# Performance work log

Hardware: AMD Instinct MI355X
Metric: run time of the kernel (lower is better)

The kernel has to match this reference:

```python
import jax, jax.numpy as jnp
import numpy as np

UP = 512      # up_size
RADIUS = 60   # revise crop radius -> 120x120 squares
COEF = 1.5    # COM threshold coefficient
DOT = 4       # intensity-adjust circle radius
B = 16
M = 4
BASE = 128


def _affine_grid(theta, H, W):
    # torch F.affine_grid, align_corners=False. theta: (2,3) -> grid (H,W,2) with (x,y)
    xs = (2.0 * jnp.arange(W, dtype=jnp.float32) + 1.0) / W - 1.0
    ys = (2.0 * jnp.arange(H, dtype=jnp.float32) + 1.0) / H - 1.0
    X, Y = jnp.meshgrid(xs, ys)  # (H,W), X varies along width
    base = jnp.stack([X, Y, jnp.ones_like(X)], axis=-1)  # (H,W,3)
    return base @ theta.T  # (H,W,2)


def _gs_one(im, gr):
    # torch F.grid_sample, bilinear, zero padding, align_corners=False
    # im: (C,H,W), gr: (Hg,Wg,2) -> (C,Hg,Wg)
    C, H, W = im.shape
    x = ((gr[..., 0] + 1.0) * W - 1.0) * 0.5
    y = ((gr[..., 1] + 1.0) * H - 1.0) * 0.5
    x0 = jnp.floor(x)
    y0 = jnp.floor(y)
    wx = x - x0
    wy = y - y0

    def tap(ix, iy, w):
        valid = (ix >= 0) & (ix < W) & (iy >= 0) & (iy < H)
        ii = jnp.clip(iy, 0, H - 1).astype(jnp.int32)
        jj = jnp.clip(ix, 0, W - 1).astype(jnp.int32)
        return im[:, ii, jj] * (jnp.where(valid, w, 0.0))[None]

    return (tap(x0, y0, (1 - wx) * (1 - wy))
            + tap(x0 + 1, y0, wx * (1 - wy))
            + tap(x0, y0 + 1, (1 - wx) * wy)
            + tap(x0 + 1, y0 + 1, wx * wy))


_grid_sample = jax.vmap(_gs_one)  # (B,C,H,W),(B,Hg,Wg,2)->(B,C,Hg,Wg)


def _inv2x3(theta):
    # append [0,0,1], invert 3x3, keep top 2 rows (as in Joint.forward)
    n = theta.shape[0]
    bottom = jnp.broadcast_to(jnp.array([[0.0, 0.0, 1.0]], jnp.float32), (n, 1, 3))
    full = jnp.concatenate([theta, bottom], axis=1)
    return jnp.linalg.inv(full)[:, :2]


def _com(img, mask, coef):
    # center_of_mass: threshold = coef * mean over mask, intensity-weighted centroid
    H, W = img.shape
    msum = jnp.maximum(mask.sum(), 1.0)
    thr = (img.sum() / msum) * coef
    w = jnp.where(img > thr, img, 0.0)
    tot = w.sum() + 1e-8
    cx = (w.sum(axis=1) * jnp.arange(H, dtype=img.dtype)).sum() / tot  # row
    cy = (w.sum(axis=0) * jnp.arange(W, dtype=img.dtype)).sum() / tot  # col
    return cx, cy


def _revise(image, masks_rot, inv_theta, adj, radius, coef, dot):
    # revise_size_on_affine_gpu with adj_para given and pare_reverse=True
    d = 2 * radius
    yy, xx = jnp.meshgrid(jnp.arange(d), jnp.arange(d), indexing='ij')
    small_sq = ((yy - radius) ** 2 + (xx - radius) ** 2) <= dot ** 2  # dot mask

    def per_item(img_i, new_i, mask_i, th_i, a_i):
        cx, cy = _com(new_i, mask_i, coef)
        x0 = jnp.round(cx).astype(jnp.int32) - radius
        y0 = jnp.round(cy).astype(jnp.int32) - radius
        small = jax.lax.dynamic_slice(img_i[0], (x0, y0), (d, d))
        small = jnp.where(small_sq, small / a_i, small)  # pare_reverse=True -> divide
        out = _gs_one(small[None], _affine_grid(th_i, d, d))  # (1,d,d)
        return jax.lax.dynamic_update_slice(img_i, out, (0, x0, y0))

    img = image
    for j in range(masks_rot.shape[0]):
        mj = masks_rot[j]                 # (B,H,W) float 0/1
        new = image[:, 0] * mj            # COM always from original image*mask
        img = jax.vmap(per_item)(img, new, mj, inv_theta, adj)
    return img


def setup_inputs() -> dict:
    key = jax.random.key(0)
    ks = jax.random.split(key, 6)
    predicted_base = jax.random.uniform(ks[0], (B, 1, BASE, BASE), jnp.float32)
    e = 0.05 * jax.random.normal(ks[1], (B, 4), jnp.float32)
    sc = (jnp.zeros((B, 2, 3), jnp.float32)
          .at[:, 0, 0].set(1.0 + e[:, 0]).at[:, 0, 1].set(e[:, 1])
          .at[:, 1, 0].set(e[:, 2]).at[:, 1, 1].set(1.0 + e[:, 3]))
    ang = jax.random.uniform(ks[2], (B,), jnp.float32, -0.2, 0.2)
    rot = (jnp.zeros((B, 2, 3), jnp.float32)
           .at[:, 0, 0].set(jnp.cos(ang)).at[:, 0, 1].set(-jnp.sin(ang))
           .at[:, 1, 0].set(jnp.sin(ang)).at[:, 1, 1].set(jnp.cos(ang)))
    t = jax.random.uniform(ks[3], (B, 2), jnp.float32, -0.05, 0.05)
    tr = (jnp.zeros((B, 2, 3), jnp.float32)
          .at[:, 0, 0].set(1.0).at[:, 1, 1].set(1.0)
          .at[:, 0, 2].set(t[:, 0]).at[:, 1, 2].set(t[:, 1]))
    adj = jax.random.uniform(ks[4], (B,), jnp.float32, 0.9, 1.1)
    centers = [(128, 128), (128, 384), (384, 128), (384, 384)]
    yy, xx = np.meshgrid(np.arange(UP), np.arange(UP), indexing='ij')
    masks = np.stack([((yy - cy) ** 2 + (xx - cx) ** 2 <= 30 ** 2).astype(np.float32)
                      for (cy, cx) in centers])
    return dict(predicted_base=predicted_base, scaler_shear=sc, rotation=rot,
                translation=tr, adj_mask=adj, masks=jnp.asarray(masks))


def reference(predicted_base, scaler_shear, rotation, translation, adj_mask, masks):
    b = predicted_base.shape[0]
    it1 = _inv2x3(scaler_shear)
    it2 = _inv2x3(rotation)
    it3 = _inv2x3(translation)
    base_inp = jax.image.resize(predicted_base, (b, 1, UP, UP), method='linear')
    mk_grid = jax.vmap(lambda th: _affine_grid(th, UP, UP))
    g1, g2, g3 = mk_grid(it1), mk_grid(it2), mk_grid(it3)
    pred_trans = _grid_sample(base_inp, g3)
    pred_rot = _grid_sample(pred_trans, g2)
    pred_input = _grid_sample(pred_rot, g1)
    # rotate masks through grid_2 then grid_1, threshold at 0.5
    new_masks = []
    for j in range(masks.shape[0]):
        bm = jnp.broadcast_to(masks[j][None, None], (b, 1, UP, UP))
        rm = _grid_sample(_grid_sample(bm, g2), g1)
        new_masks.append(rm[:, 0] >= 0.5)
    masks_rot = jnp.stack(new_masks)  # (M,B,UP,UP) bool
    pred_revise = _revise(pred_input, masks_rot.astype(pred_input.dtype), it1,
                          adj_mask, RADIUS, COEF, DOT)
    return (base_inp, pred_input, pred_revise, masks_rot)
```

## Files before the change

kernel.cpp:

```cpp
#include <hip/hip_runtime.h>
#include <math.h>
#include <limits.h>

#define NPIX (512*512)
#define NB 16
#define RAD 60
#define DSZ 120
#define PSTR 121
#define GTS 48
#define GSTR 49


__device__ __forceinline__ float gs_bilinear(const float* img, int H, int W,
                                             float gx, float gy) {
    float x = ((gx + 1.0f) * (float)W - 1.0f) * 0.5f;
    float y = ((gy + 1.0f) * (float)H - 1.0f) * 0.5f;
    float xf = floorf(x), yf = floorf(y);
    int ix = (int)xf, iy = (int)yf;
    float wx = x - xf, wy = y - yf;
    float v = 0.0f;
    bool vx0 = (ix >= 0) && (ix < W);
    bool vx1 = (ix >= -1) && (ix < W - 1);
    bool vy0 = (iy >= 0) && (iy < H);
    bool vy1 = (iy >= -1) && (iy < H - 1);
    if (vx0 && vy0) v += img[iy*W + ix]         * ((1.0f - wx) * (1.0f - wy));
    if (vx1 && vy0) v += img[iy*W + ix + 1]     * (wx * (1.0f - wy));
    if (vx0 && vy1) v += img[(iy+1)*W + ix]     * ((1.0f - wx) * wy);
    if (vx1 && vy1) v += img[(iy+1)*W + ix + 1] * (wx * wy);
    return v;
}

__device__ __forceinline__ float gs_bilinear_patch(const float* img, float gx, float gy) {
    float x = ((gx + 1.0f) * 120.0f - 1.0f) * 0.5f;
    float y = ((gy + 1.0f) * 120.0f - 1.0f) * 0.5f;
    float xf = floorf(x), yf = floorf(y);
    int ix = (int)xf, iy = (int)yf;
    float wx = x - xf, wy = y - yf;
    float v = 0.0f;
    bool vx0 = (ix >= 0) && (ix < 120);
    bool vx1 = (ix >= -1) && (ix < 119);
    bool vy0 = (iy >= 0) && (iy < 120);
    bool vy1 = (iy >= -1) && (iy < 119);
    if (vx0 && vy0) v += img[iy*PSTR + ix]         * ((1.0f - wx) * (1.0f - wy));
    if (vx1 && vy0) v += img[iy*PSTR + ix + 1]     * (wx * (1.0f - wy));
    if (vx0 && vy1) v += img[(iy+1)*PSTR + ix]     * ((1.0f - wx) * wy);
    if (vx1 && vy1) v += img[(iy+1)*PSTR + ix + 1] * (wx * wy);
    return v;
}


__global__ void k_prep(const float* __restrict__ sc, const float* __restrict__ rot,
                       const float* __restrict__ tr, float* __restrict__ ws_inv,
                       int* __restrict__ bbox, unsigned* __restrict__ occ,
                       int* __restrict__ qcount) {
    int t = threadIdx.x;
    if (t < 48) {
        int m = t >> 4, b = t & 15;
        const float* th = (m == 0 ? sc : (m == 1 ? rot : tr)) + b * 6;
        float a  = th[0], bb = th[1], tx = th[2];
        float c  = th[3], d  = th[4], ty = th[5];
        float L10 = c / a;
        float dp  = d  - L10 * bb;
        float typ = ty - L10 * tx;
        float i10 = (0.0f - L10) / dp;
        float i00 = (1.0f - bb * i10) / a;
        float i11 = 1.0f / dp;
        float i01 = (0.0f - bb * i11) / a;
        float i12 = (0.0f - typ) / dp;
        float i02 = (0.0f - bb * i12 - tx) / a;
        float* o = ws_inv + m * 96 + b * 6;
        o[0] = i00; o[1] = i01; o[2] = i02;
        o[3] = i10; o[4] = i11; o[5] = i12;
    }
    bbox[t] = ((t & 3) < 2) ? INT_MAX : INT_MIN;
    if (t < 128) occ[t] = 0u;
    if (t == 0) *qcount = 0;
}

__global__ void __launch_bounds__(256) k_occ(const float* __restrict__ masks,
                                             unsigned* __restrict__ occ) {
    int tile = blockIdx.x * 4 + (threadIdx.x >> 6);
    int lane = threadIdx.x & 63;
    int j = tile >> 10, t = tile & 1023;
    int ty = t >> 5, tx = t & 31;
    const float* mk = masks + (size_t)j * NPIX;
    int any = 0;
    for (int i = lane; i < 256; i += 64) {
        int py = ty * 16 + (i >> 4), px = tx * 16 + (i & 15);
        if (mk[py * 512 + px] != 0.0f) any = 1;
    }
    unsigned long long m = __ballot(any);
    if (lane == 0 && m) atomicOr(&occ[j * 32 + ty], 1u << tx);
}

__global__ void __launch_bounds__(256) k_otile(const unsigned* __restrict__ occ,
                                               const float* __restrict__ inv1,
                                               const float* __restrict__ inv2,
                                               int* __restrict__ queue,
                                               int* __restrict__ qcount) {
    int idx = blockIdx.x * 256 + threadIdx.x;
    int jb = idx >> 10, tile = idx & 1023;
    int j = jb >> 4, b = jb & 15;
    int ty = tile >> 5, tx = tile & 31;
    const float* t1 = inv1 + b * 6;
    const float* t2 = inv2 + b * 6;
    float xs[2] = { (float)(tx * 16), (float)(tx * 16 + 15) };
    float ys[2] = { (float)(ty * 16), (float)(ty * 16 + 15) };
    float sxmin = 1e30f, sxmax = -1e30f, symin = 1e30f, symax = -1e30f;
    for (int cy = 0; cy < 2; ++cy)
        for (int cx = 0; cx < 2; ++cx) {
            float X = (2.0f * xs[cx] + 1.0f) / 512.0f - 1.0f;
            float Y = (2.0f * ys[cy] + 1.0f) / 512.0f - 1.0f;
            float gx = t1[0] * X + t1[1] * Y + t1[2];
            float gy = t1[3] * X + t1[4] * Y + t1[5];
            float sx = ((gx + 1.0f) * 512.0f - 1.0f) * 0.5f;
            float sy = ((gy + 1.0f) * 512.0f - 1.0f) * 0.5f;
            sxmin = fminf(sxmin, sx); sxmax = fmaxf(sxmax, sx);
            symin = fminf(symin, sy); symax = fmaxf(symax, sy);
        }
    int c0 = max((int)floorf(sxmin) - 1, 0), c1 = min((int)floorf(sxmax) + 2, 511);
    int r0 = max((int)floorf(symin) - 1, 0), r1 = min((int)floorf(symax) + 2, 511);
    bool any = false;
    if (c0 <= c1 && r0 <= r1) {
        float A0 = t2[0], A1 = t2[1], A3 = t2[3], A4 = t2[4];
        float Kx = 0.5f * (-511.0f * (A0 + A1) + 512.0f * t2[2] + 511.0f);
        float Ky = 0.5f * (-511.0f * (A3 + A4) + 512.0f * t2[5] + 511.0f);
        float pxmin = A0 * (A0 >= 0.f ? c0 : c1) + A1 * (A1 >= 0.f ? r0 : r1) + Kx;
        float pxmax = A0 * (A0 >= 0.f ? c1 : c0) + A1 * (A1 >= 0.f ? r1 : r0) + Kx;
        float pymin = A3 * (A3 >= 0.f ? c0 : c1) + A4 * (A4 >= 0.f ? r0 : r1) + Ky;
        float pymax = A3 * (A3 >= 0.f ? c1 : c0) + A4 * (A4 >= 0.f ? r1 : r0) + Ky;
        int xlo = max((int)floorf(pxmin) - 1, 0), xhi = min((int)floorf(pxmax) + 2, 511);
        int ylo = max((int)floorf(pymin) - 1, 0), yhi = min((int)floorf(pymax) + 2, 511);
        if (xlo <= xhi && ylo <= yhi)
            for (int tr = ylo >> 4; tr <= yhi >> 4; ++tr)
                for (int tc = xlo >> 4; tc <= xhi >> 4; ++tc)
                    if ((occ[j * 32 + tr] >> tc) & 1u) any = true;
    }
    if (any) {
        int pos = atomicAdd(qcount, 1);
        queue[pos] = (jb << 10) | tile;
    }
}

__global__ void __launch_bounds__(256) k_zero(float4* __restrict__ p, int n4) {
    int stride = gridDim.x * 256;
    for (int i = blockIdx.x * 256 + threadIdx.x; i < n4; i += stride)
        p[i] = make_float4(0.f, 0.f, 0.f, 0.f);
}

__global__ void __launch_bounds__(256) k_upsample(const float* __restrict__ in,
                                                  float* __restrict__ out) {
    int b = blockIdx.y;
    int p4 = blockIdx.x * 256 + threadIdx.x;
    int p = p4 * 4;
    int y = p >> 9, x0p = p & 511;
    const float* src = in + b * 128 * 128;
    float r[4];
    float sy = (float)y * 0.25f - 0.375f;
    float fy0 = floorf(sy);
    int iy = (int)fy0;
    float fy = sy - fy0;
    int iy0 = min(max(iy, 0), 127), iy1 = min(max(iy + 1, 0), 127);
    #pragma unroll
    for (int k = 0; k < 4; ++k) {
        int x = x0p + k;
        float sx = (float)x * 0.25f - 0.375f;
        float fx0 = floorf(sx);
        int ix = (int)fx0;
        float fx = sx - fx0;
        int ix0 = min(max(ix, 0), 127), ix1 = min(max(ix + 1, 0), 127);
        float v00 = src[iy0 * 128 + ix0], v10 = src[iy0 * 128 + ix1];
        float v01 = src[iy1 * 128 + ix0], v11 = src[iy1 * 128 + ix1];
        r[k] = (v00 * (1.0f - fx) + v10 * fx) * (1.0f - fy)
             + (v01 * (1.0f - fx) + v11 * fx) * fy;
    }
    *(float4*)(out + (size_t)b * NPIX + p) = make_float4(r[0], r[1], r[2], r[3]);
}

__global__ void __launch_bounds__(256) k_gsample(const float* __restrict__ src,
                                                 float* __restrict__ dst,
                                                 float* __restrict__ dst2,
                                                 const float* __restrict__ thetas) {
    __shared__ float tb[GTS * GSTR];
    int b = blockIdx.y;
    int tile = blockIdx.x;
    int ox = (tile & 15) * 32, oy = (tile >> 4) * 32;
    const float* th = thetas + b * 6;
    float t0 = th[0], t1 = th[1], t2 = th[2], t3 = th[3], t4 = th[4], t5 = th[5];
    const float* im = src + (size_t)b * NPIX;

    float sxmin = 1e30f, sxmax = -1e30f, symin = 1e30f, symax = -1e30f;
    #pragma unroll
    for (int cy = 0; cy < 2; ++cy)
        #pragma unroll
        for (int cx = 0; cx < 2; ++cx) {
            float X = (2.0f * (float)(ox + cx * 31) + 1.0f) / 512.0f - 1.0f;
            float Y = (2.0f * (float)(oy + cy * 31) + 1.0f) / 512.0f - 1.0f;
            float gx = t0 * X + t1 * Y + t2;
            float gy = t3 * X + t4 * Y + t5;
            float sx = ((gx + 1.0f) * 512.0f - 1.0f) * 0.5f;
            float sy = ((gy + 1.0f) * 512.0f - 1.0f) * 0.5f;
            sxmin = fminf(sxmin, sx); sxmax = fmaxf(sxmax, sx);
            symin = fminf(symin, sy); symax = fmaxf(symax, sy);
        }
    int rx0 = (int)floorf(sxmin) - 1;
    int ry0 = (int)floorf(symin) - 1;
    bool fits = ((int)floorf(sxmax) + 2 - rx0 < GTS) &&
                ((int)floorf(symax) + 2 - ry0 < GTS);

    int t = threadIdx.x;
    int py = oy + (t >> 3);
    int px0 = ox + (t & 7) * 4;
    float Y = (2.0f * (float)py + 1.0f) / 512.0f - 1.0f;
    float r[4];

    if (fits) {
        for (int i = t; i < GTS * GTS; i += 256) {
            int rr = i / GTS, cc = i - rr * GTS;
            int gy_ = ry0 + rr, gx_ = rx0 + cc;
            float v = 0.0f;
            if (gx_ >= 0 && gx_ < 512 && gy_ >= 0 && gy_ < 512)
                v = im[gy_ * 512 + gx_];
            tb[rr * GSTR + cc] = v;
        }
        __syncthreads();
        #pragma unroll
        for (int k = 0; k < 4; ++k) {
            float X = (2.0f * (float)(px0 + k) + 1.0f) / 512.0f - 1.0f;
            float gx = t0 * X + t1 * Y + t2;
            float gy = t3 * X + t4 * Y + t5;
            float x = ((gx + 1.0f) * 512.0f - 1.0f) * 0.5f;
            float y = ((gy + 1.0f) * 512.0f - 1.0f) * 0.5f;
            float xf = floorf(x), yf = floorf(y);
            int ix = (int)xf, iy = (int)yf;
            float wx = x - xf, wy = y - yf;
            int lx = ix - rx0, ly = iy - ry0;
            float v;
            v  = tb[ly * GSTR + lx]           * ((1.0f - wx) * (1.0f - wy));
            v += tb[ly * GSTR + lx + 1]       * (wx * (1.0f - wy));
            v += tb[(ly + 1) * GSTR + lx]     * ((1.0f - wx) * wy);
            v += tb[(ly + 1) * GSTR + lx + 1] * (wx * wy);
            r[k] = v;
        }
    } else {
        #pragma unroll
        for (int k = 0; k < 4; ++k) {
            float X = (2.0f * (float)(px0 + k) + 1.0f) / 512.0f - 1.0f;
            float gx = t0 * X + t1 * Y + t2;
            float gy = t3 * X + t4 * Y + t5;
            r[k] = gs_bilinear(im, 512, 512, gx, gy);
        }
    }
    float4 v4 = make_float4(r[0], r[1], r[2], r[3]);
    size_t op = (size_t)b * NPIX + py * 512 + px0;
    *(float4*)(dst + op) = v4;
    if (dst2) *(float4*)(dst2 + op) = v4;
}

__device__ __forceinline__ float rm2_val(const float* mk, const float* t2, int cx_, int ry_) {
    float X2 = (2.0f * (float)cx_ + 1.0f) / 512.0f - 1.0f;
    float Y2 = (2.0f * (float)ry_ + 1.0f) / 512.0f - 1.0f;
    float g2x = t2[0] * X2 + t2[1] * Y2 + t2[2];
    float g2y = t2[3] * X2 + t2[4] * Y2 + t2[5];
    return gs_bilinear(mk, 512, 512, g2x, g2y);
}

__global__ void __launch_bounds__(256) k_mask_live(const float* __restrict__ masks,
                                                   float* __restrict__ out3,
                                                   const float* __restrict__ inv1,
                                                   const float* __restrict__ inv2,
                                                   const int* __restrict__ queue,
                                                   const int* __restrict__ qcount,
                                                   int* __restrict__ bbox) {
    __shared__ int sbb[4];
    int n = *qcount;
    for (int q = blockIdx.x; q < n; q += gridDim.x) {
        int e = queue[q];
        int jb = e >> 10, tile = e & 1023;
        if (threadIdx.x == 0) { sbb[0] = INT_MAX; sbb[1] = INT_MAX; sbb[2] = INT_MIN; sbb[3] = INT_MIN; }
        __syncthreads();

        int ty = tile >> 5, tx = tile & 31;
        int y = ty * 16 + (threadIdx.x >> 4);
        int x = tx * 16 + (threadIdx.x & 15);
        int j = jb >> 4, b = jb & 15;
        const float* t1 = inv1 + b * 6;
        const float* t2 = inv2 + b * 6;
        const float* mk = masks + (size_t)j * NPIX;

        float X = (2.0f * (float)x + 1.0f) / 512.0f - 1.0f;
        float Y = (2.0f * (float)y + 1.0f) / 512.0f - 1.0f;
        float gx = t1[0] * X + t1[1] * Y + t1[2];
        float gy = t1[3] * X + t1[4] * Y + t1[5];
        float sx = ((gx + 1.0f) * 512.0f - 1.0f) * 0.5f;
        float sy = ((gy + 1.0f) * 512.0f - 1.0f) * 0.5f;
        float xf = floorf(sx), yf = floorf(sy);
        int ix = (int)xf, iy = (int)yf;
        float wx = sx - xf, wy = sy - yf;

        float v = 0.0f;
        bool vx0 = (ix >= 0) && (ix < 512);
        bool vx1 = (ix >= -1) && (ix < 511);
        bool vy0 = (iy >= 0) && (iy < 512);
        bool vy1 = (iy >= -1) && (iy < 511);
        if (vx0 && vy0) v += rm2_val(mk, t2, ix,     iy    ) * ((1.0f - wx) * (1.0f - wy));
        if (vx1 && vy0) v += rm2_val(mk, t2, ix + 1, iy    ) * (wx * (1.0f - wy));
        if (vx0 && vy1) v += rm2_val(mk, t2, ix,     iy + 1) * ((1.0f - wx) * wy);
        if (vx1 && vy1) v += rm2_val(mk, t2, ix + 1, iy + 1) * (wx * wy);

        float res = 0.0f;
        if (v >= 0.5f) {
            res = 1.0f;
            atomicMin(&sbb[0], y); atomicMin(&sbb[1], x);
            atomicMax(&sbb[2], y); atomicMax(&sbb[3], x);
        }
        out3[(size_t)jb * NPIX + y * 512 + x] = res;

        __syncthreads();
        if (threadIdx.x == 0 && sbb[2] != INT_MIN) {
            atomicMin(&bbox[jb * 4 + 0], sbb[0]);
            atomicMin(&bbox[jb * 4 + 1], sbb[1]);
            atomicMax(&bbox[jb * 4 + 2], sbb[2]);
            atomicMax(&bbox[jb * 4 + 3], sbb[3]);
        }
        __syncthreads();
    }
}

__global__ void __launch_bounds__(256) k_stats(const float* __restrict__ pred,
                                               const float* __restrict__ mrot,
                                               const int* __restrict__ bbox,
                                               int* __restrict__ xy) {
    int jb = blockIdx.x;
    int b = jb & 15;
    int rmin = bbox[jb*4+0], cmin = bbox[jb*4+1], rmax = bbox[jb*4+2], cmax = bbox[jb*4+3];
    const float* img = pred + (size_t)b * NPIX;
    const float* mk  = mrot + (size_t)jb * NPIX;
    int lane = threadIdx.x & 63, w = threadIdx.x >> 6;
    int W = cmax - cmin + 1;
    int total = (rmax >= rmin) ? W * (rmax - rmin + 1) : 0;

    double msum = 0.0, isum = 0.0;
    for (int i = threadIdx.x; i < total; i += 256) {
        int r = rmin + i / W, c = cmin + i % W;
        float m = mk[r * 512 + c];
        if (m != 0.0f) {
            msum += (double)m;
            isum += (double)(img[r * 512 + c] * m);
        }
    }
    for (int o = 32; o > 0; o >>= 1) {
        msum += __shfl_down(msum, o, 64);
        isum += __shfl_down(isum, o, 64);
    }
    __shared__ double s0[4], s1[4], s2[4];
    __shared__ double sthr;
    if (lane == 0) { s0[w] = msum; s1[w] = isum; }
    __syncthreads();
    if (threadIdx.x == 0) {
        double M = s0[0] + s0[1] + s0[2] + s0[3];
        double I = s1[0] + s1[1] + s1[2] + s1[3];
        sthr = (I / fmax(M, 1.0)) * 1.5;
    }
    __syncthreads();
    double t = sthr;

    double wsum = 0.0, sy = 0.0, sx = 0.0;
    for (int i = threadIdx.x; i < total; i += 256) {
        int r = rmin + i / W, c = cmin + i % W;
        float m = mk[r * 512 + c];
        if (m != 0.0f) {
            float v = img[r * 512 + c] * m;
            if ((double)v > t) {
                double vd = (double)v;
                wsum += vd;
                sy += vd * (double)r;
                sx += vd * (double)c;
            }
        }
    }
    for (int o = 32; o > 0; o >>= 1) {
        wsum += __shfl_down(wsum, o, 64);
        sy   += __shfl_down(sy,   o, 64);
        sx   += __shfl_down(sx,   o, 64);
    }
    __syncthreads();
    if (lane == 0) { s0[w] = wsum; s1[w] = sy; s2[w] = sx; }
    __syncthreads();
    if (threadIdx.x == 0) {
        double W_ = s0[0] + s0[1] + s0[2] + s0[3];
        double SY = s1[0] + s1[1] + s1[2] + s1[3];
        double SX = s2[0] + s2[1] + s2[2] + s2[3];
        double tot = W_ + 1e-8;
        int x0 = (int)rint(SY / tot) - RAD;
        int y0 = (int)rint(SX / tot) - RAD;
        x0 = min(max(x0, 0), 512 - DSZ);
        y0 = min(max(y0, 0), 512 - DSZ);
        xy[jb * 2 + 0] = x0;
        xy[jb * 2 + 1] = y0;
    }
}

__device__ __forceinline__ void patch_one(float* __restrict__ im, float* __restrict__ patch,
                                          int x0, int y0, float a,
                                          float t0, float t1, float t2,
                                          float t3, float t4, float t5) {
    for (int t = threadIdx.x; t < DSZ * DSZ; t += 1024) {
        int u = t / DSZ, v = t % DSZ;
        float val = im[(x0 + u) * 512 + (y0 + v)];
        int du = u - RAD, dv = v - RAD;
        if (du * du + dv * dv <= 16) val = val / a;
        patch[u * PSTR + v] = val;
    }
    __syncthreads();
    for (int t = threadIdx.x; t < DSZ * DSZ; t += 1024) {
        int py = t / DSZ, px = t % DSZ;
        float X = (2.0f * (float)px + 1.0f) / 120.0f - 1.0f;
        float Y = (2.0f * (float)py + 1.0f) / 120.0f - 1.0f;
        float gx = t0 * X + t1 * Y + t2;
        float gy = t3 * X + t4 * Y + t5;
        float o = gs_bilinear_patch(patch, gx, gy);
        im[(x0 + py) * 512 + (y0 + px)] = o;
    }
}

__global__ void __launch_bounds__(1024) k_patch(float* __restrict__ img,
                                                const int* __restrict__ xy,
                                                const float* __restrict__ inv1,
                                                const float* __restrict__ adj) {
    __shared__ float patch[DSZ * PSTR];
    int b = blockIdx.x >> 2, j = blockIdx.x & 3;
    int rx[4], ry[4];
    #pragma unroll
    for (int k = 0; k < 4; ++k) {
        rx[k] = xy[(k * 16 + b) * 2 + 0];
        ry[k] = xy[(k * 16 + b) * 2 + 1];
    }
    bool overlap = false;
    #pragma unroll
    for (int i = 0; i < 4; ++i)
        #pragma unroll
        for (int k = 0; k < 4; ++k)
            if (i < k && abs(rx[i] - rx[k]) < DSZ && abs(ry[i] - ry[k]) < DSZ)
                overlap = true;

    float a = adj[b];
    float* im = img + (size_t)b * NPIX;
    const float* th = inv1 + b * 6;
    float t0 = th[0], t1 = th[1], t2 = th[2], t3 = th[3], t4 = th[4], t5 = th[5];

    if (!overlap) {
        patch_one(im, patch, rx[j], ry[j], a, t0, t1, t2, t3, t4, t5);
    } else {
        if (j != 0) return;
        for (int jj = 0; jj < 4; ++jj) {
            patch_one(im, patch, rx[jj], ry[jj], a, t0, t1, t2, t3, t4, t5);
            __threadfence_block();
            __syncthreads();
        }
    }
}


extern "C" void kernel_launch(void* const* d_in, const int* in_sizes, int n_in,
                              void* d_out, int out_size, void* d_ws, size_t ws_size,
                              hipStream_t stream) {
    const float* base  = (const float*)d_in[0];
    const float* sc    = (const float*)d_in[1];
    const float* rot   = (const float*)d_in[2];
    const float* tr    = (const float*)d_in[3];
    const float* adj   = (const float*)d_in[4];
    const float* masks = (const float*)d_in[5];

    float* out  = (float*)d_out;
    float* out0 = out;
    float* out1 = out0 + (size_t)NB * NPIX;
    float* out2 = out1 + (size_t)NB * NPIX;
    float* out3 = out2 + (size_t)NB * NPIX;

    float*    inv1   = (float*)d_ws;
    float*    inv2   = inv1 + 96;
    float*    inv3   = inv1 + 192;
    int*      xy     = (int*)((char*)d_ws + 4096);
    int*      bbox   = (int*)((char*)d_ws + 8192);
    unsigned* occ    = (unsigned*)((char*)d_ws + 12288);
    int*      qcount = (int*)((char*)d_ws + 16128);
    int*      queue  = (int*)((char*)d_ws + 16384);

    dim3 gridUp(256, NB);
    dim3 gridTile(256, NB);

    k_prep<<<1, 256, 0, stream>>>(sc, rot, tr, (float*)d_ws, bbox, occ, qcount);
    k_occ<<<1024, 256, 0, stream>>>(masks, occ);
    k_otile<<<256, 256, 0, stream>>>(occ, inv1, inv2, queue, qcount);
    k_upsample<<<gridUp, 256, 0, stream>>>(base, out0);

    k_gsample<<<gridTile, 256, 0, stream>>>(out0, out2, nullptr, inv3);
    k_gsample<<<gridTile, 256, 0, stream>>>(out2, out3, nullptr, inv2);
    k_gsample<<<gridTile, 256, 0, stream>>>(out3, out1, out2, inv1);

    k_zero<<<2048, 256, 0, stream>>>((float4*)out3, 64 * NPIX / 4);
    k_mask_live<<<1024, 256, 0, stream>>>(masks, out3, inv1, inv2, queue, qcount, bbox);

    k_stats<<<64, 256, 0, stream>>>(out1, out3, bbox, xy);

    k_patch<<<64, 1024, 0, stream>>>(out2, xy, inv1, adj);
}
```

Baseline: 247.0 us.

## Merge prep, occupancy, upsample and tile-queue kernels; skip zeroing live mask tiles

Combines the independent setup work (theta inversion, mask occupancy bitmap, upsampling) into one kernel split by block index, and puts the output-tile liveness test into the first grid-sample launch. Occupancy words are now built with one vectorized wave per row instead of per-tile atomics. The zero-fill is merged with the live-mask kernel and writes only tiles that no live block will overwrite, using a new per-tile flag array. This cuts the launch count from about eleven to seven and removes redundant zero writes to the mask output, in exchange for branchy mixed-role kernels and an extra byte-flag array.

```diff
diff --git a/kernel.cpp b/kernel.cpp
--- a/kernel.cpp
+++ b/kernel.cpp
@@ -48,57 +48,181 @@
     return v;
 }
 
-
-__global__ void k_prep(const float* __restrict__ sc, const float* __restrict__ rot,
-                       const float* __restrict__ tr, float* __restrict__ ws_inv,
-                       int* __restrict__ bbox, unsigned* __restrict__ occ,
-                       int* __restrict__ qcount) {
+__global__ void __launch_bounds__(256) k_init(const float* __restrict__ base,
+                                              const float* __restrict__ sc,
+                                              const float* __restrict__ rot,
+                                              const float* __restrict__ tr,
+                                              const float* __restrict__ masks,
+                                              float* __restrict__ out0,
+                                              float* __restrict__ ws_inv,
+                                              int* __restrict__ bbox,
+                                              unsigned* __restrict__ occ,
+                                              int* __restrict__ qcount) {
+    int bid = blockIdx.x;
+    if (bid < 4096) {
+        int b = bid >> 8;
+        int p4 = (bid & 255) * 256 + threadIdx.x;
+        int p = p4 * 4;
+        int y = p >> 9, x0p = p & 511;
+        const float* src = base + b * 128 * 128;
+        float r[4];
+        float sy = (float)y * 0.25f - 0.375f;
+        float fy0 = floorf(sy);
+        int iy = (int)fy0;
+        float fy = sy - fy0;
+        int iy0 = min(max(iy, 0), 127), iy1 = min(max(iy + 1, 0), 127);
+        #pragma unroll
+        for (int k = 0; k < 4; ++k) {
+            int x = x0p + k;
+            float sx = (float)x * 0.25f - 0.375f;
+            float fx0 = floorf(sx);
+            int ix = (int)fx0;
+            float fx = sx - fx0;
+            int ix0 = min(max(ix, 0), 127), ix1 = min(max(ix + 1, 0), 127);
+            float v00 = src[iy0 * 128 + ix0], v10 = src[iy0 * 128 + ix1];
+            float v01 = src[iy1 * 128 + ix0], v11 = src[iy1 * 128 + ix1];
+            r[k] = (v00 * (1.0f - fx) + v10 * fx) * (1.0f - fy)
+                 + (v01 * (1.0f - fx) + v11 * fx) * fy;
+        }
+        *(float4*)(out0 + (size_t)b * NPIX + p) = make_float4(r[0], r[1], r[2], r[3]);
+    } else if (bid < 4128) {
+        int word = (bid - 4096) * 4 + (threadIdx.x >> 6);
+        int lane = threadIdx.x & 63;
+        int j = word >> 5, ty = word & 31;
+        const float* mk = masks + (size_t)j * NPIX + ty * 16 * 512 + lane * 8;
+        int any = 0;
+        for (int rr = 0; rr < 16; ++rr) {
+            const float4* p = (const float4*)(mk + rr * 512);
+            float4 a = p[0], c = p[1];
+            if (a.x != 0.f || a.y != 0.f || a.z != 0.f || a.w != 0.f ||
+                c.x != 0.f || c.y != 0.f || c.z != 0.f || c.w != 0.f) any = 1;
+        }
+        unsigned long long bb = __ballot(any);
+        if (lane == 0) {
+            unsigned wrd = 0;
+            for (int tx = 0; tx < 32; ++tx)
+                if (bb & (3ull << (2 * tx))) wrd |= 1u << tx;
+            occ[j * 32 + ty] = wrd;
+        }
+    } else {
+        int t = threadIdx.x;
+        if (t < 48) {
+            int m = t >> 4, b = t & 15;
+            const float* th = (m == 0 ? sc : (m == 1 ? rot : tr)) + b * 6;
+            float a  = th[0], bbv = th[1], tx = th[2];
+            float c  = th[3], d   = th[4], ty = th[5];
+            float L10 = c / a;
+            float dp  = d  - L10 * bbv;
+            float typ = ty - L10 * tx;
+            float i10 = (0.0f - L10) / dp;
+            float i00 = (1.0f - bbv * i10) / a;
+            float i11 = 1.0f / dp;
+            float i01 = (0.0f - bbv * i11) / a;
+            float i12 = (0.0f - typ) / dp;
+            float i02 = (0.0f - bbv * i12 - tx) / a;
+            float* o = ws_inv + m * 96 + b * 6;
+            o[0] = i00; o[1] = i01; o[2] = i02;
+            o[3] = i10; o[4] = i11; o[5] = i12;
+        }
+        bbox[t] = ((t & 3) < 2) ? INT_MAX : INT_MIN;
+        if (t == 0) *qcount = 0;
+    }
+}
+
+__device__ __forceinline__ void gsample_tile(const float* __restrict__ src,
+                                             float* __restrict__ dst,
+                                             float* __restrict__ dst2,
+                                             const float* __restrict__ thetas,
+                                             int b, int tile, float* tb) {
+    int ox = (tile & 15) * 32, oy = (tile >> 4) * 32;
+    const float* th = thetas + b * 6;
+    float t0 = th[0], t1 = th[1], t2 = th[2], t3 = th[3], t4 = th[4], t5 = th[5];
+    const float* im = src + (size_t)b * NPIX;
+
+    float sxmin = 1e30f, sxmax = -1e30f, symin = 1e30f, symax = -1e30f;
+    #pragma unroll
+    for (int cy = 0; cy < 2; ++cy)
+        #pragma unroll
+        for (int cx = 0; cx < 2; ++cx) {
+            float X = (2.0f * (float)(ox + cx * 31) + 1.0f) / 512.0f - 1.0f;
+            float Y = (2.0f * (float)(oy + cy * 31) + 1.0f) / 512.0f - 1.0f;
+            float gx = t0 * X + t1 * Y + t2;
+            float gy = t3 * X + t4 * Y + t5;
+            float sx = ((gx + 1.0f) * 512.0f - 1.0f) * 0.5f;
+            float sy = ((gy + 1.0f) * 512.0f - 1.0f) * 0.5f;
+            sxmin = fminf(sxmin, sx); sxmax = fmaxf(sxmax, sx);
+            symin = fminf(symin, sy); symax = fmaxf(symax, sy);
+        }
+    int rx0 = (int)floorf(sxmin) - 1;
+    int ry0 = (int)floorf(symin) - 1;
+    bool fits = ((int)floorf(sxmax) + 2 - rx0 < GTS) &&
+                ((int)floorf(symax) + 2 - ry0 < GTS);
+
     int t = threadIdx.x;
-    if (t < 48) {
-        int m = t >> 4, b = t & 15;
-        const float* th = (m == 0 ? sc : (m == 1 ? rot : tr)) + b * 6;
-        float a  = th[0], bb = th[1], tx = th[2];
-        float c  = th[3], d  = th[4], ty = th[5];
-        float L10 = c / a;
-        float dp  = d  - L10 * bb;
-        float typ = ty - L10 * tx;
-        float i10 = (0.0f - L10) / dp;
-        float i00 = (1.0f - bb * i10) / a;
-        float i11 = 1.0f / dp;
-        float i01 = (0.0f - bb * i11) / a;
-        float i12 = (0.0f - typ) / dp;
-        float i02 = (0.0f - bb * i12 - tx) / a;
-        float* o = ws_inv + m * 96 + b * 6;
-        o[0] = i00; o[1] = i01; o[2] = i02;
-        o[3] = i10; o[4] = i11; o[5] = i12;
-    }
-    bbox[t] = ((t & 3) < 2) ? INT_MAX : INT_MIN;
-    if (t < 128) occ[t] = 0u;
-    if (t == 0) *qcount = 0;
-}
-
-__global__ void __launch_bounds__(256) k_occ(const float* __restrict__ masks,
-                                             unsigned* __restrict__ occ) {
-    int tile = blockIdx.x * 4 + (threadIdx.x >> 6);
-    int lane = threadIdx.x & 63;
-    int j = tile >> 10, t = tile & 1023;
-    int ty = t >> 5, tx = t & 31;
-    const float* mk = masks + (size_t)j * NPIX;
-    int any = 0;
-    for (int i = lane; i < 256; i += 64) {
-        int py = ty * 16 + (i >> 4), px = tx * 16 + (i & 15);
-        if (mk[py * 512 + px] != 0.0f) any = 1;
-    }
-    unsigned long long m = __ballot(any);
-    if (lane == 0 && m) atomicOr(&occ[j * 32 + ty], 1u << tx);
-}
-
-__global__ void __launch_bounds__(256) k_otile(const unsigned* __restrict__ occ,
-                                               const float* __restrict__ inv1,
-                                               const float* __restrict__ inv2,
-                                               int* __restrict__ queue,
-                                               int* __restrict__ qcount) {
-    int idx = blockIdx.x * 256 + threadIdx.x;
+    int py = oy + (t >> 3);
+    int px0 = ox + (t & 7) * 4;
+    float Y = (2.0f * (float)py + 1.0f) / 512.0f - 1.0f;
+    float r[4];
+
+    if (fits) {
+        for (int i = t; i < GTS * GTS; i += 256) {
+            int rr = i / GTS, cc = i - rr * GTS;
+            int gy_ = ry0 + rr, gx_ = rx0 + cc;
+            float v = 0.0f;
+            if (gx_ >= 0 && gx_ < 512 && gy_ >= 0 && gy_ < 512)
+                v = im[gy_ * 512 + gx_];
+            tb[rr * GSTR + cc] = v;
+        }
+        __syncthreads();
+        #pragma unroll
+        for (int k = 0; k < 4; ++k) {
+            float X = (2.0f * (float)(px0 + k) + 1.0f) / 512.0f - 1.0f;
+            float gx = t0 * X + t1 * Y + t2;
+            float gy = t3 * X + t4 * Y + t5;
+            float x = ((gx + 1.0f) * 512.0f - 1.0f) * 0.5f;
+            float y = ((gy + 1.0f) * 512.0f - 1.0f) * 0.5f;
+            float xf = floorf(x), yf = floorf(y);
+            int ix = (int)xf, iy = (int)yf;
+            float wx = x - xf, wy = y - yf;
+            int lx = ix - rx0, ly = iy - ry0;
+            float v;
+            v  = tb[ly * GSTR + lx]           * ((1.0f - wx) * (1.0f - wy));
+            v += tb[ly * GSTR + lx + 1]       * (wx * (1.0f - wy));
+            v += tb[(ly + 1) * GSTR + lx]     * ((1.0f - wx) * wy);
+            v += tb[(ly + 1) * GSTR + lx + 1] * (wx * wy);
+            r[k] = v;
+        }
+    } else {
+        #pragma unroll
+        for (int k = 0; k < 4; ++k) {
+            float X = (2.0f * (float)(px0 + k) + 1.0f) / 512.0f - 1.0f;
+            float gx = t0 * X + t1 * Y + t2;
+            float gy = t3 * X + t4 * Y + t5;
+            r[k] = gs_bilinear(im, 512, 512, gx, gy);
+        }
+    }
+    float4 v4 = make_float4(r[0], r[1], r[2], r[3]);
+    size_t op = (size_t)b * NPIX + py * 512 + px0;
+    *(float4*)(dst + op) = v4;
+    if (dst2) *(float4*)(dst2 + op) = v4;
+}
+
+__global__ void __launch_bounds__(256) k_g3ot(const float* __restrict__ src,
+                                              float* __restrict__ dst,
+                                              const float* __restrict__ inv3,
+                                              const unsigned* __restrict__ occ,
+                                              const float* __restrict__ inv1,
+                                              const float* __restrict__ inv2,
+                                              unsigned char* __restrict__ otile,
+                                              int* __restrict__ queue,
+                                              int* __restrict__ qcount) {
+    __shared__ float tb[GTS * GSTR];
+    int bid = blockIdx.x;
+    if (bid < 4096) {
+        gsample_tile(src, dst, nullptr, inv3, bid >> 8, bid & 255, tb);
+        return;
+    }
+    int idx = (bid - 4096) * 256 + threadIdx.x;
     int jb = idx >> 10, tile = idx & 1023;
     int j = jb >> 4, b = jb & 15;
     int ty = tile >> 5, tx = tile & 31;
@@ -136,45 +260,11 @@
                 for (int tc = xlo >> 4; tc <= xhi >> 4; ++tc)
                     if ((occ[j * 32 + tr] >> tc) & 1u) any = true;
     }
+    otile[idx] = any ? 1 : 0;
     if (any) {
         int pos = atomicAdd(qcount, 1);
         queue[pos] = (jb << 10) | tile;
     }
-}
-
-__global__ void __launch_bounds__(256) k_zero(float4* __restrict__ p, int n4) {
-    int stride = gridDim.x * 256;
-    for (int i = blockIdx.x * 256 + threadIdx.x; i < n4; i += stride)
-        p[i] = make_float4(0.f, 0.f, 0.f, 0.f);
-}
-
-__global__ void __launch_bounds__(256) k_upsample(const float* __restrict__ in,
-                                                  float* __restrict__ out) {
-    int b = blockIdx.y;
-    int p4 = blockIdx.x * 256 + threadIdx.x;
-    int p = p4 * 4;
-    int y = p >> 9, x0p = p & 511;
-    const float* src = in + b * 128 * 128;
-    float r[4];
-    float sy = (float)y * 0.25f - 0.375f;
-    float fy0 = floorf(sy);
-    int iy = (int)fy0;
-    float fy = sy - fy0;
-    int iy0 = min(max(iy, 0), 127), iy1 = min(max(iy + 1, 0), 127);
-    #pragma unroll
-    for (int k = 0; k < 4; ++k) {
-        int x = x0p + k;
-        float sx = (float)x * 0.25f - 0.375f;
-        float fx0 = floorf(sx);
-        int ix = (int)fx0;
-        float fx = sx - fx0;
-        int ix0 = min(max(ix, 0), 127), ix1 = min(max(ix + 1, 0), 127);
-        float v00 = src[iy0 * 128 + ix0], v10 = src[iy0 * 128 + ix1];
-        float v01 = src[iy1 * 128 + ix0], v11 = src[iy1 * 128 + ix1];
-        r[k] = (v00 * (1.0f - fx) + v10 * fx) * (1.0f - fy)
-             + (v01 * (1.0f - fx) + v11 * fx) * fy;
-    }
-    *(float4*)(out + (size_t)b * NPIX + p) = make_float4(r[0], r[1], r[2], r[3]);
 }
 
 __global__ void __launch_bounds__(256) k_gsample(const float* __restrict__ src,
@@ -182,79 +272,7 @@
                                                  float* __restrict__ dst2,
                                                  const float* __restrict__ thetas) {
     __shared__ float tb[GTS * GSTR];
-    int b = blockIdx.y;
-    int tile = blockIdx.x;
-    int ox = (tile & 15) * 32, oy = (tile >> 4) * 32;
-    const float* th = thetas + b * 6;
-    float t0 = th[0], t1 = th[1], t2 = th[2], t3 = th[3], t4 = th[4], t5 = th[5];
-    const float* im = src + (size_t)b * NPIX;
-
-    float sxmin = 1e30f, sxmax = -1e30f, symin = 1e30f, symax = -1e30f;
-    #pragma unroll
-    for (int cy = 0; cy < 2; ++cy)
-        #pragma unroll
-        for (int cx = 0; cx < 2; ++cx) {
-            float X = (2.0f * (float)(ox + cx * 31) + 1.0f) / 512.0f - 1.0f;
-            float Y = (2.0f * (float)(oy + cy * 31) + 1.0f) / 512.0f - 1.0f;
-            float gx = t0 * X + t1 * Y + t2;
-            float gy = t3 * X + t4 * Y + t5;
-            float sx = ((gx + 1.0f) * 512.0f - 1.0f) * 0.5f;
-            float sy = ((gy + 1.0f) * 512.0f - 1.0f) * 0.5f;
-            sxmin = fminf(sxmin, sx); sxmax = fmaxf(sxmax, sx);
-            symin = fminf(symin, sy); symax = fmaxf(symax, sy);
-        }
-    int rx0 = (int)floorf(sxmin) - 1;
-    int ry0 = (int)floorf(symin) - 1;
-    bool fits = ((int)floorf(sxmax) + 2 - rx0 < GTS) &&
-                ((int)floorf(symax) + 2 - ry0 < GTS);
-
-    int t = threadIdx.x;
-    int py = oy + (t >> 3);
-    int px0 = ox + (t & 7) * 4;
-    float Y = (2.0f * (float)py + 1.0f) / 512.0f - 1.0f;
-    float r[4];
-
-    if (fits) {
-        for (int i = t; i < GTS * GTS; i += 256) {
-            int rr = i / GTS, cc = i - rr * GTS;
-            int gy_ = ry0 + rr, gx_ = rx0 + cc;
-            float v = 0.0f;
-            if (gx_ >= 0 && gx_ < 512 && gy_ >= 0 && gy_ < 512)
-                v = im[gy_ * 512 + gx_];
-            tb[rr * GSTR + cc] = v;
-        }
-        __syncthreads();
-        #pragma unroll
-        for (int k = 0; k < 4; ++k) {
-            float X = (2.0f * (float)(px0 + k) + 1.0f) / 512.0f - 1.0f;
-            float gx = t0 * X + t1 * Y + t2;
-            float gy = t3 * X + t4 * Y + t5;
-            float x = ((gx + 1.0f) * 512.0f - 1.0f) * 0.5f;
-            float y = ((gy + 1.0f) * 512.0f - 1.0f) * 0.5f;
-            float xf = floorf(x), yf = floorf(y);
-            int ix = (int)xf, iy = (int)yf;
-            float wx = x - xf, wy = y - yf;
-            int lx = ix - rx0, ly = iy - ry0;
-            float v;
-            v  = tb[ly * GSTR + lx]           * ((1.0f - wx) * (1.0f - wy));
-            v += tb[ly * GSTR + lx + 1]       * (wx * (1.0f - wy));
-            v += tb[(ly + 1) * GSTR + lx]     * ((1.0f - wx) * wy);
-            v += tb[(ly + 1) * GSTR + lx + 1] * (wx * wy);
-            r[k] = v;
-        }
-    } else {
-        #pragma unroll
-        for (int k = 0; k < 4; ++k) {
-            float X = (2.0f * (float)(px0 + k) + 1.0f) / 512.0f - 1.0f;
-            float gx = t0 * X + t1 * Y + t2;
-            float gy = t3 * X + t4 * Y + t5;
-            r[k] = gs_bilinear(im, 512, 512, gx, gy);
-        }
-    }
-    float4 v4 = make_float4(r[0], r[1], r[2], r[3]);
-    size_t op = (size_t)b * NPIX + py * 512 + px0;
-    *(float4*)(dst + op) = v4;
-    if (dst2) *(float4*)(dst2 + op) = v4;
+    gsample_tile(src, dst, dst2, thetas, blockIdx.x >> 8, blockIdx.x & 255, tb);
 }
 
 __device__ __forceinline__ float rm2_val(const float* mk, const float* t2, int cx_, int ry_) {
@@ -265,16 +283,32 @@
     return gs_bilinear(mk, 512, 512, g2x, g2y);
 }
 
-__global__ void __launch_bounds__(256) k_mask_live(const float* __restrict__ masks,
-                                                   float* __restrict__ out3,
-                                                   const float* __restrict__ inv1,
-                                                   const float* __restrict__ inv2,
-                                                   const int* __restrict__ queue,
-                                                   const int* __restrict__ qcount,
-                                                   int* __restrict__ bbox) {
+__global__ void __launch_bounds__(256) k_zml(const float* __restrict__ masks,
+                                             float* __restrict__ out3,
+                                             const float* __restrict__ inv1,
+                                             const float* __restrict__ inv2,
+                                             const unsigned char* __restrict__ otile,
+                                             const int* __restrict__ queue,
+                                             const int* __restrict__ qcount,
+                                             int* __restrict__ bbox) {
+    int bid = blockIdx.x;
+    if (bid < 2048) {
+        const float4 z4 = make_float4(0.f, 0.f, 0.f, 0.f);
+        float4* p = (float4*)out3;
+        int stride = 2048 * 256;
+        for (int i = bid * 256 + threadIdx.x; i < 64 * NPIX / 4; i += stride) {
+            int jb = i >> 16;
+            int w = i & 65535;
+            int y = w >> 7;
+            int x = (w << 2) & 511;
+            int tile = ((y >> 4) << 5) | (x >> 4);
+            if (!otile[(jb << 10) | tile]) p[i] = z4;
+        }
+        return;
+    }
     __shared__ int sbb[4];
     int n = *qcount;
-    for (int q = blockIdx.x; q < n; q += gridDim.x) {
+    for (int q = bid - 2048; q < n; q += 1024) {
         int e = queue[q];
         int jb = e >> 10, tile = e & 1023;
         if (threadIdx.x == 0) { sbb[0] = INT_MAX; sbb[1] = INT_MAX; sbb[2] = INT_MIN; sbb[3] = INT_MIN; }
@@ -478,31 +512,23 @@
     float* out2 = out1 + (size_t)NB * NPIX;
     float* out3 = out2 + (size_t)NB * NPIX;
 
-    float*    inv1   = (float*)d_ws;
-    float*    inv2   = inv1 + 96;
-    float*    inv3   = inv1 + 192;
-    int*      xy     = (int*)((char*)d_ws + 4096);
-    int*      bbox   = (int*)((char*)d_ws + 8192);
-    unsigned* occ    = (unsigned*)((char*)d_ws + 12288);
-    int*      qcount = (int*)((char*)d_ws + 16128);
-    int*      queue  = (int*)((char*)d_ws + 16384);
-
-    dim3 gridUp(256, NB);
-    dim3 gridTile(256, NB);
-
-    k_prep<<<1, 256, 0, stream>>>(sc, rot, tr, (float*)d_ws, bbox, occ, qcount);
-    k_occ<<<1024, 256, 0, stream>>>(masks, occ);
-    k_otile<<<256, 256, 0, stream>>>(occ, inv1, inv2, queue, qcount);
-    k_upsample<<<gridUp, 256, 0, stream>>>(base, out0);
-
-    k_gsample<<<gridTile, 256, 0, stream>>>(out0, out2, nullptr, inv3);
-    k_gsample<<<gridTile, 256, 0, stream>>>(out2, out3, nullptr, inv2);
-    k_gsample<<<gridTile, 256, 0, stream>>>(out3, out1, out2, inv1);
-
-    k_zero<<<2048, 256, 0, stream>>>((float4*)out3, 64 * NPIX / 4);
-    k_mask_live<<<1024, 256, 0, stream>>>(masks, out3, inv1, inv2, queue, qcount, bbox);
-
+    float*         inv1   = (float*)d_ws;
+    float*         inv2   = inv1 + 96;
+    float*         inv3   = inv1 + 192;
+    int*           xy     = (int*)((char*)d_ws + 4096);
+    int*           bbox   = (int*)((char*)d_ws + 8192);
+    unsigned*      occ    = (unsigned*)((char*)d_ws + 12288);
+    int*           qcount = (int*)((char*)d_ws + 16128);
+    unsigned char* otile  = (unsigned char*)((char*)d_ws + 16384);
+    int*           queue  = (int*)((char*)d_ws + 81920);
+
+    k_init<<<4129, 256, 0, stream>>>(base, sc, rot, tr, masks, out0,
+                                     (float*)d_ws, bbox, occ, qcount);
+    k_g3ot<<<4352, 256, 0, stream>>>(out0, out2, inv3, occ, inv1, inv2,
+                                     otile, queue, qcount);
+    k_gsample<<<4096, 256, 0, stream>>>(out2, out3, nullptr, inv2);
+    k_gsample<<<4096, 256, 0, stream>>>(out3, out1, out2, inv1);
+    k_zml<<<3072, 256, 0, stream>>>(masks, out3, inv1, inv2, otile, queue, qcount, bbox);
     k_stats<<<64, 256, 0, stream>>>(out1, out3, bbox, xy);
-
     k_patch<<<64, 1024, 0, stream>>>(out2, xy, inv1, adj);
 }
```

Measured after the change: 246.6 us. No clear change (-0.2%).
